# Kernel tuning notes

Measured on AMD Instinct MI355X. Metric: run time of the kernel, lower is better.

Reference implementation:

```python
import jax, jax.numpy as jnp
import numpy as np

NEG_SLOPE = 0.2


def _gat_layer(x, src, dst, W, att_s, att_d, bias):
    # x: [N, F_in]; W: [F_in, H*C]; att_s/att_d: [H, C]; bias: [H*C]
    N = x.shape[0]
    H, C = att_s.shape
    h = (x @ W).reshape(N, H, C)                      # projected features [N,H,C]
    a_src = jnp.einsum('nhc,hc->nh', h, att_s)        # [N,H] per-node src logits
    a_dst = jnp.einsum('nhc,hc->nh', h, att_d)        # [N,H]
    e = a_src[src] + a_dst[dst]                       # [E,H] edge logits
    e = jnp.where(e > 0, e, NEG_SLOPE * e)            # leaky_relu
    # scatter-softmax over incoming edges of each destination node
    m = jax.ops.segment_max(e, dst, num_segments=N)   # [N,H]
    ex = jnp.exp(e - m[dst])                          # [E,H]
    denom = jax.ops.segment_sum(ex, dst, num_segments=N)  # [N,H]
    alpha = ex / denom[dst]                           # [E,H]
    # scatter-add aggregation of weighted source features
    msg = h[src] * alpha[:, :, None]                  # [E,H,C]
    out = jax.ops.segment_sum(msg, dst, num_segments=N)   # [N,H,C]
    return out.reshape(N, H * C) + bias


def _with_self_loops(edge_index, N):
    loop = jnp.arange(N, dtype=edge_index.dtype)
    src = jnp.concatenate([edge_index[0], loop])
    dst = jnp.concatenate([edge_index[1], loop])
    return src, dst


def setup_inputs() -> dict:
    key = jax.random.key(0)
    ks = jax.random.split(key, 10)
    N, E = 50000, 800000
    F_in, C1, H1, F_out = 128, 64, 4, 128
    x = jax.random.normal(ks[0], (N, F_in), dtype=jnp.float32)
    edge_index = jax.random.randint(ks[1], (2, E), 0, N, dtype=jnp.int64)
    s1 = 1.0 / np.sqrt(F_in)
    W1 = jax.random.normal(ks[2], (F_in, H1 * C1), dtype=jnp.float32) * s1
    att_src1 = jax.random.normal(ks[3], (H1, C1), dtype=jnp.float32) * 0.1
    att_dst1 = jax.random.normal(ks[4], (H1, C1), dtype=jnp.float32) * 0.1
    bias1 = jnp.zeros((H1 * C1,), dtype=jnp.float32)
    s2 = 1.0 / np.sqrt(H1 * C1)
    W2 = jax.random.normal(ks[5], (H1 * C1, F_out), dtype=jnp.float32) * s2
    att_src2 = jax.random.normal(ks[6], (1, F_out), dtype=jnp.float32) * 0.1
    att_dst2 = jax.random.normal(ks[7], (1, F_out), dtype=jnp.float32) * 0.1
    bias2 = jnp.zeros((F_out,), dtype=jnp.float32)
    return {"x": x, "edge_index": edge_index,
            "W1": W1, "att_src1": att_src1, "att_dst1": att_dst1, "bias1": bias1,
            "W2": W2, "att_src2": att_src2, "att_dst2": att_dst2, "bias2": bias2}


def reference(x, edge_index, W1, att_src1, att_dst1, bias1,
              W2, att_src2, att_dst2, bias2):
    N = x.shape[0]
    src, dst = _with_self_loops(edge_index, N)
    h1 = _gat_layer(x, src, dst, W1, att_src1, att_dst1, bias1)
    h1 = jax.nn.elu(h1)
    out = _gat_layer(h1, src, dst, W2, att_src2, att_dst2, bias2)
    return out
```

## Files before the change

### kernel.cpp

```cpp
#include <hip/hip_runtime.h>

#define NN 50000
#define NE 800000

constexpr int H1 = 4, F1 = 128, HC1 = 256;
constexpr int HC2 = 128;

typedef unsigned short u16;
typedef unsigned int u32;
typedef __attribute__((ext_vector_type(8))) short bf16x8;
typedef __attribute__((ext_vector_type(4))) float f32x4;

__device__ __forceinline__ float bf2f(u16 h) {
    return __uint_as_float(((u32)h) << 16);
}
__device__ __forceinline__ u16 f2bf(float f) {
    u32 u = __float_as_uint(f);
    u32 r = (u + 0x7fffu + ((u >> 16) & 1u)) >> 16;
    return (u16)r;
}

__device__ __forceinline__ int ld_edge(const int* e32, const long long* e64, int is64, long long idx) {
    return is64 ? (int)e64[idx] : e32[idx];
}

__global__ __launch_bounds__(256) void k_cvt(const float* __restrict__ in, u16* __restrict__ out, int n8) {
    int i = blockIdx.x * 256 + threadIdx.x;
    if (i >= n8) return;
    const float4* p = (const float4*)in + (size_t)i * 2;
    float4 a = p[0], b = p[1];
    ushort4 o0, o1;
    o0.x = f2bf(a.x); o0.y = f2bf(a.y); o0.z = f2bf(a.z); o0.w = f2bf(a.w);
    o1.x = f2bf(b.x); o1.y = f2bf(b.y); o1.z = f2bf(b.z); o1.w = f2bf(b.w);
    ((ushort4*)out)[(size_t)i * 2] = o0;
    ((ushort4*)out)[(size_t)i * 2 + 1] = o1;
}

__global__ void k_zero_detect(int* __restrict__ p, const int* __restrict__ e32, int* __restrict__ flag) {
    int i = blockIdx.x * blockDim.x + threadIdx.x;
    if (i < NN) p[i] = 0;
    if (i == 0) {
        int z = 1;
        for (int t = 0; t < 16; t++)
            if (e32[2 * t + 1] != 0) z = 0;
        *flag = z;
    }
}

__global__ void k_count(const int* __restrict__ e32, const long long* __restrict__ e64,
                        const int* __restrict__ flag, int* __restrict__ deg) {
    int e = blockIdx.x * blockDim.x + threadIdx.x;
    if (e >= NE) return;
    int is64 = *flag;
    int dst = ld_edge(e32, e64, is64, (long long)NE + e);
    atomicAdd(&deg[dst], 1);
}

__global__ __launch_bounds__(256) void k_part(const int* __restrict__ deg, int* __restrict__ bsum) {
    int i = blockIdx.x * 256 + threadIdx.x;
    int v = (i < NN) ? deg[i] : 0;
    #pragma unroll
    for (int off = 1; off < 64; off <<= 1) v += __shfl_xor(v, off);
    __shared__ int ws[4];
    if ((threadIdx.x & 63) == 0) ws[threadIdx.x >> 6] = v;
    __syncthreads();
    if (threadIdx.x == 0) bsum[blockIdx.x] = ws[0] + ws[1] + ws[2] + ws[3];
}

__global__ __launch_bounds__(256) void k_scanb(const int* __restrict__ bsum, int* __restrict__ boff,
                                               int* __restrict__ row_ptr, int NB) {
    const int tid = threadIdx.x;
    const int lane = tid & 63, wv = tid >> 6;
    int v = (tid < NB) ? bsum[tid] : 0;
    int x = v;
    #pragma unroll
    for (int off = 1; off < 64; off <<= 1) {
        int t = __shfl_up(x, off);
        if (lane >= off) x += t;
    }
    __shared__ int wsum[4], woff[4];
    if (lane == 63) wsum[wv] = x;
    __syncthreads();
    if (tid == 0) {
        int run = 0;
        #pragma unroll
        for (int j = 0; j < 4; j++) { woff[j] = run; run += wsum[j]; }
        row_ptr[NN] = run;
    }
    __syncthreads();
    if (tid < NB) boff[tid] = x - v + woff[wv];
}

__global__ __launch_bounds__(256) void k_addb(const int* __restrict__ deg, const int* __restrict__ boff,
                                              int* __restrict__ row_ptr, int* __restrict__ cursor) {
    const int tid = threadIdx.x;
    const int lane = tid & 63, wv = tid >> 6;
    int i = blockIdx.x * 256 + tid;
    int v = (i < NN) ? deg[i] : 0;
    int x = v;
    #pragma unroll
    for (int off = 1; off < 64; off <<= 1) {
        int t = __shfl_up(x, off);
        if (lane >= off) x += t;
    }
    __shared__ int wsum[4], woff[4];
    if (lane == 63) wsum[wv] = x;
    __syncthreads();
    if (tid == 0) {
        int run = 0;
        #pragma unroll
        for (int j = 0; j < 4; j++) { woff[j] = run; run += wsum[j]; }
    }
    __syncthreads();
    int excl = x - v + woff[wv] + boff[blockIdx.x];
    if (i < NN) { row_ptr[i] = excl; cursor[i] = excl; }
}

__global__ void k_fill(const int* __restrict__ e32, const long long* __restrict__ e64,
                       const int* __restrict__ flag, int* __restrict__ cursor, int* __restrict__ col) {
    int e = blockIdx.x * blockDim.x + threadIdx.x;
    if (e >= NE) return;
    int is64 = *flag;
    int src = ld_edge(e32, e64, is64, e);
    int dst = ld_edge(e32, e64, is64, (long long)NE + e);
    int pos = atomicAdd(&cursor[dst], 1);
    col[pos] = src;
}

template <int K, int N>
__global__ __launch_bounds__(256) void k_prepw(const float* __restrict__ W, u16* __restrict__ Wp) {
    constexpr int LGN = (N == 256) ? 8 : 7;
    int o = blockIdx.x * 256 + threadIdx.x;
    if (o >= K * N) return;
    int j = o & 7;
    int lk = (o >> 3) & 3;
    int nn = (o >> 5) & (N - 1);
    int kc = o >> (5 + LGN);
    int k = kc * 32 + lk * 8 + j;
    Wp[o] = f2bf(W[(size_t)k * N + nn]);
}

template <int K, int NOUT, int HEADS, int TPB>
__global__ __launch_bounds__(TPB) void k_gemm_mfma(
    const u16* __restrict__ Ab, const u16* __restrict__ Wp,
    const float* __restrict__ atts, const float* __restrict__ attd,
    u16* __restrict__ Hout, float* __restrict__ as_out, float* __restrict__ ad_out, int M)
{
    constexpr int BM = 64, BK = 32;
    constexpr int NK = K / BK;
    constexpr int C = NOUT / HEADS;
    constexpr int LDA = 40;
    __shared__ __align__(16) u16 As[2][BM * LDA];
    __shared__ float red_s[BM * HEADS];
    __shared__ float red_d[BM * HEADS];

    const int tid = threadIdx.x;
    const int w = tid >> 6;
    const int l = tid & 63;
    const int l15 = l & 15, lk = l >> 4;
    const int row0 = blockIdx.x * BM;
    const int col0 = w * 64;

    for (int i = tid; i < BM * HEADS; i += TPB) { red_s[i] = 0.f; red_d[i] = 0.f; }

    f32x4 acc[4][4];
    #pragma unroll
    for (int rt = 0; rt < 4; rt++)
        #pragma unroll
        for (int nt = 0; nt < 4; nt++)
            acc[rt][nt] = (f32x4){0.f, 0.f, 0.f, 0.f};

    auto stage = [&](int kc, int b) {
        #pragma unroll
        for (int i = tid; i < BM * 4; i += TPB) {
            int r = i >> 2, c = (i & 3) * 8;
            int gr = row0 + r;
            bf16x8 v = {0, 0, 0, 0, 0, 0, 0, 0};
            if (gr < M) v = *(const bf16x8*)(Ab + (size_t)gr * K + kc * BK + c);
            *(bf16x8*)&As[b][r * LDA + c] = v;
        }
    };
    auto loadB = [&](int kc, bf16x8* bf) {
        #pragma unroll
        for (int nt = 0; nt < 4; nt++)
            bf[nt] = *(const bf16x8*)(Wp + (((size_t)kc * NOUT + col0 + nt * 16 + l15) * 4 + lk) * 8);
    };

    bf16x8 bcur[4];
    loadB(0, bcur);
    stage(0, 0);
    for (int kc = 0; kc < NK; ++kc) {
        __syncthreads();
        bf16x8 afr[4];
        #pragma unroll
        for (int rt = 0; rt < 4; rt++)
            afr[rt] = *(const bf16x8*)&As[kc & 1][(rt * 16 + l15) * LDA + lk * 8];
        bf16x8 bnext[4];
        if (kc + 1 < NK) {
            loadB(kc + 1, bnext);
            stage(kc + 1, (kc + 1) & 1);
        }
        #pragma unroll
        for (int rt = 0; rt < 4; rt++)
            #pragma unroll
            for (int nt = 0; nt < 4; nt++)
                acc[rt][nt] = __builtin_amdgcn_mfma_f32_16x16x32_bf16(afr[rt], bcur[nt], acc[rt][nt], 0, 0, 0);
        if (kc + 1 < NK) {
            #pragma unroll
            for (int nt = 0; nt < 4; nt++) bcur[nt] = bnext[nt];
        }
    }

    #pragma unroll
    for (int rt = 0; rt < 4; rt++) {
        #pragma unroll
        for (int t = 0; t < 4; t++) {
            int gr = row0 + rt * 16 + lk * 4 + t;
            if (gr < M) {
                #pragma unroll
                for (int nt = 0; nt < 4; nt++)
                    Hout[(size_t)gr * NOUT + col0 + nt * 16 + l15] = f2bf(acc[rt][nt][t]);
            }
        }
    }

    float avs[4], avd[4];
    #pragma unroll
    for (int nt = 0; nt < 4; nt++) {
        int gc = col0 + nt * 16 + l15;
        avs[nt] = atts[gc];
        avd[nt] = attd[gc];
    }
    const int headw = col0 / C;
    #pragma unroll
    for (int rt = 0; rt < 4; rt++) {
        #pragma unroll
        for (int t = 0; t < 4; t++) {
            float ps = 0.f, pd = 0.f;
            #pragma unroll
            for (int nt = 0; nt < 4; nt++) {
                ps = fmaf(acc[rt][nt][t], avs[nt], ps);
                pd = fmaf(acc[rt][nt][t], avd[nt], pd);
            }
            ps += __shfl_xor(ps, 1); ps += __shfl_xor(ps, 2);
            ps += __shfl_xor(ps, 4); ps += __shfl_xor(ps, 8);
            pd += __shfl_xor(pd, 1); pd += __shfl_xor(pd, 2);
            pd += __shfl_xor(pd, 4); pd += __shfl_xor(pd, 8);
            if (l15 == 0) {
                int row = rt * 16 + lk * 4 + t;
                atomicAdd(&red_s[row * HEADS + headw], ps);
                atomicAdd(&red_d[row * HEADS + headw], pd);
            }
        }
    }
    __syncthreads();
    for (int i = tid; i < BM * HEADS; i += TPB) {
        int gr = row0 + i / HEADS;
        if (gr < M) {
            as_out[(size_t)gr * HEADS + i % HEADS] = red_s[i];
            ad_out[(size_t)gr * HEADS + i % HEADS] = red_d[i];
        }
    }
}

__global__ __launch_bounds__(256) void k_agg1(
    const int* __restrict__ row_ptr, const int* __restrict__ col,
    const u16* __restrict__ Hb, const float* __restrict__ as_, const float* __restrict__ ad_,
    const float* __restrict__ bias, u16* __restrict__ outp)
{
    __shared__ int    s_src[4][64];
    __shared__ float4 s_p[4][64];
    int n = blockIdx.x * 4 + (threadIdx.x >> 6);
    if (n >= NN) return;
    const int lane = threadIdx.x & 63;
    const int wv = threadIdx.x >> 6;
    const int head = lane >> 4;
    float4 ad4 = *(const float4*)(ad_ + (size_t)n * 4);
    int beg = row_ptr[n];
    int cnt = row_ptr[n + 1] - beg + 1;
    float4 sp = make_float4(0.f, 0.f, 0.f, 0.f);
    float ax = 0.f, ay = 0.f, az = 0.f, aw = 0.f;
    for (int c = 0; c < cnt; c += 64) {
        int idx = c + lane;
        int srcl = n;
        float4 p4 = make_float4(0.f, 0.f, 0.f, 0.f);
        if (idx < cnt) {
            srcl = (idx == 0) ? n : col[beg + idx - 1];
            float4 a4 = *(const float4*)(as_ + (size_t)srcl * 4);
            float e;
            e = a4.x + ad4.x; e = e > 0.f ? e : 0.2f * e; p4.x = __expf(e);
            e = a4.y + ad4.y; e = e > 0.f ? e : 0.2f * e; p4.y = __expf(e);
            e = a4.z + ad4.z; e = e > 0.f ? e : 0.2f * e; p4.z = __expf(e);
            e = a4.w + ad4.w; e = e > 0.f ? e : 0.2f * e; p4.w = __expf(e);
        }
        sp.x += p4.x; sp.y += p4.y; sp.z += p4.z; sp.w += p4.w;
        s_src[wv][lane] = srcl;
        s_p[wv][lane] = p4;
        int jmax = min(64, cnt - c);
        #pragma unroll 4
        for (int j = 0; j < jmax; ++j) {
            int srcj = s_src[wv][j];
            float pj = ((const float*)&s_p[wv][j])[head];
            ushort4 hv = *(const ushort4*)(Hb + (size_t)srcj * HC1 + lane * 4);
            ax = fmaf(pj, bf2f(hv.x), ax);
            ay = fmaf(pj, bf2f(hv.y), ay);
            az = fmaf(pj, bf2f(hv.z), az);
            aw = fmaf(pj, bf2f(hv.w), aw);
        }
    }
    #pragma unroll
    for (int off = 1; off < 64; off <<= 1) {
        sp.x += __shfl_xor(sp.x, off);
        sp.y += __shfl_xor(sp.y, off);
        sp.z += __shfl_xor(sp.z, off);
        sp.w += __shfl_xor(sp.w, off);
    }
    float s = head < 2 ? (head == 0 ? sp.x : sp.y) : (head == 2 ? sp.z : sp.w);
    float inv = 1.f / s;
    float4 bv = *(const float4*)(bias + lane * 4);
    float4 o;
    o.x = ax * inv + bv.x;
    o.y = ay * inv + bv.y;
    o.z = az * inv + bv.z;
    o.w = aw * inv + bv.w;
    o.x = o.x > 0.f ? o.x : __expf(o.x) - 1.f;
    o.y = o.y > 0.f ? o.y : __expf(o.y) - 1.f;
    o.z = o.z > 0.f ? o.z : __expf(o.z) - 1.f;
    o.w = o.w > 0.f ? o.w : __expf(o.w) - 1.f;
    ushort4 ob;
    ob.x = f2bf(o.x); ob.y = f2bf(o.y); ob.z = f2bf(o.z); ob.w = f2bf(o.w);
    *(ushort4*)(outp + (size_t)n * HC1 + lane * 4) = ob;
}

__global__ __launch_bounds__(256) void k_agg2(
    const int* __restrict__ row_ptr, const int* __restrict__ col,
    const u16* __restrict__ Hb, const float* __restrict__ as_, const float* __restrict__ ad_,
    const float* __restrict__ bias, float* __restrict__ outp)
{
    __shared__ int   s_src[4][64];
    __shared__ float s_p[4][64];
    int n = blockIdx.x * 4 + (threadIdx.x >> 6);
    if (n >= NN) return;
    const int lane = threadIdx.x & 63;
    const int wv = threadIdx.x >> 6;
    float ad0 = ad_[n];
    int beg = row_ptr[n];
    int cnt = row_ptr[n + 1] - beg + 1;
    float sp = 0.f;
    float ax = 0.f, ay = 0.f;
    for (int c = 0; c < cnt; c += 64) {
        int idx = c + lane;
        int srcl = n;
        float p = 0.f;
        if (idx < cnt) {
            srcl = (idx == 0) ? n : col[beg + idx - 1];
            float e = as_[srcl] + ad0;
            e = e > 0.f ? e : 0.2f * e;
            p = __expf(e);
        }
        sp += p;
        s_src[wv][lane] = srcl;
        s_p[wv][lane] = p;
        int jmax = min(64, cnt - c);
        #pragma unroll 4
        for (int j = 0; j < jmax; ++j) {
            int srcj = s_src[wv][j];
            float pj = s_p[wv][j];
            ushort2 hv = *(const ushort2*)(Hb + (size_t)srcj * HC2 + lane * 2);
            ax = fmaf(pj, bf2f(hv.x), ax);
            ay = fmaf(pj, bf2f(hv.y), ay);
        }
    }
    #pragma unroll
    for (int off = 1; off < 64; off <<= 1) sp += __shfl_xor(sp, off);
    float inv = 1.f / sp;
    float2 bv = *(const float2*)(bias + lane * 2);
    float2 o = make_float2(ax * inv + bv.x, ay * inv + bv.y);
    *(float2*)(outp + (size_t)n * HC2 + lane * 2) = o;
}

extern "C" void kernel_launch(void* const* d_in, const int* in_sizes, int n_in,
                              void* d_out, int out_size, void* d_ws, size_t ws_size,
                              hipStream_t stream) {
    const float* x   = (const float*)d_in[0];
    const int*       e32 = (const int*)d_in[1];
    const long long* e64 = (const long long*)d_in[1];
    const float* W1  = (const float*)d_in[2];
    const float* as1w = (const float*)d_in[3];
    const float* ad1w = (const float*)d_in[4];
    const float* b1  = (const float*)d_in[5];
    const float* W2  = (const float*)d_in[6];
    const float* as2w = (const float*)d_in[7];
    const float* ad2w = (const float*)d_in[8];
    const float* b2  = (const float*)d_in[9];
    float* out = (float*)d_out;

    char* w = (char*)d_ws;
    auto carve = [&](size_t bytes) -> void* {
        void* p = (void*)w;
        w += (bytes + 255) & ~(size_t)255;
        return p;
    };
    int*   flag    = (int*)carve(4);
    int*   row_ptr = (int*)carve((NN + 1) * sizeof(int));
    int*   cursor  = (int*)carve(NN * sizeof(int));
    int*   col     = (int*)carve(NE * sizeof(int));
    int*   bsum    = (int*)carve(256 * sizeof(int));
    int*   boff    = (int*)carve(256 * sizeof(int));
    float* as1     = (float*)carve((size_t)NN * H1 * sizeof(float));
    float* ad1     = (float*)carve((size_t)NN * H1 * sizeof(float));
    float* as2     = (float*)carve((size_t)NN * sizeof(float));
    float* ad2     = (float*)carve((size_t)NN * sizeof(float));
    u16*   xb      = (u16*)carve((size_t)NN * F1 * sizeof(u16));
    u16*   h1b     = (u16*)carve((size_t)NN * HC1 * sizeof(u16));
    u16*   h2in    = (u16*)carve((size_t)NN * HC1 * sizeof(u16));
    u16*   h2b     = (u16*)carve((size_t)NN * HC2 * sizeof(u16));
    u16*   wp1     = (u16*)carve((size_t)F1 * HC1 * sizeof(u16));
    u16*   wp2     = (u16*)carve((size_t)HC1 * HC2 * sizeof(u16));

    const int TPB = 256;
    const int gN  = (NN + TPB - 1) / TPB;
    const int gE  = (NE + TPB - 1) / TPB;
    const int gM  = (NN + 63) / 64;
    const int gAgg = (NN + 3) / 4;

    k_cvt<<<(NN * F1 / 8 + 255) / 256, 256, 0, stream>>>(x, xb, NN * F1 / 8);
    k_prepw<F1, HC1><<<F1 * HC1 / 256, 256, 0, stream>>>(W1, wp1);
    k_prepw<HC1, HC2><<<HC1 * HC2 / 256, 256, 0, stream>>>(W2, wp2);

    k_zero_detect<<<gN, TPB, 0, stream>>>(cursor, e32, flag);
    k_count<<<gE, TPB, 0, stream>>>(e32, e64, flag, cursor);
    k_part<<<gN, TPB, 0, stream>>>(cursor, bsum);
    k_scanb<<<1, 256, 0, stream>>>(bsum, boff, row_ptr, gN);
    k_addb<<<gN, TPB, 0, stream>>>(cursor, boff, row_ptr, cursor);
    k_fill<<<gE, TPB, 0, stream>>>(e32, e64, flag, cursor, col);

    k_gemm_mfma<F1, HC1, H1, 256><<<gM, 256, 0, stream>>>(xb, wp1, as1w, ad1w, h1b, as1, ad1, NN);
    k_agg1<<<gAgg, TPB, 0, stream>>>(row_ptr, col, h1b, as1, ad1, b1, h2in);

    k_gemm_mfma<HC1, HC2, 1, 128><<<gM, 128, 0, stream>>>(h2in, wp2, as2w, ad2w, h2b, as2, ad2, NN);
    k_agg2<<<gAgg, TPB, 0, stream>>>(row_ptr, col, h2b, as2, ad2, b2, out);
}
```

Before: 240.5 us.

## Slice projected features into 32-channel tables and fold self-loops into CSR

The GEMM now writes projected features in a sliced layout of 32-channel tables, each [NN][32]. Aggregation kernels are merged into one template that runs a block per (node group, slice) and processes 8 edges at once per wavefront with sub-lanes, then reduces across sub-groups. Self-loops are now stored directly in the CSR by having the degree start at 1 and writing each node's own id first, which removes the idx==0 branch. This aims to raise gather parallelism and improve cache locality per slice, at the cost of recomputing softmax logits once per slice and adding more blocks plus cross-lane reductions.

```diff
diff --git a/kernel.cpp b/kernel.cpp
--- a/kernel.cpp
+++ b/kernel.cpp
@@ -38,7 +38,7 @@
 
 __global__ void k_zero_detect(int* __restrict__ p, const int* __restrict__ e32, int* __restrict__ flag) {
     int i = blockIdx.x * blockDim.x + threadIdx.x;
-    if (i < NN) p[i] = 0;
+    if (i < NN) p[i] = 1;
     if (i == 0) {
         int z = 1;
         for (int t = 0; t < 16; t++)
@@ -92,7 +92,8 @@
 }
 
 __global__ __launch_bounds__(256) void k_addb(const int* __restrict__ deg, const int* __restrict__ boff,
-                                              int* __restrict__ row_ptr, int* __restrict__ cursor) {
+                                              int* __restrict__ row_ptr, int* __restrict__ cursor,
+                                              int* __restrict__ col) {
     const int tid = threadIdx.x;
     const int lane = tid & 63, wv = tid >> 6;
     int i = blockIdx.x * 256 + tid;
@@ -113,7 +114,11 @@
     }
     __syncthreads();
     int excl = x - v + woff[wv] + boff[blockIdx.x];
-    if (i < NN) { row_ptr[i] = excl; cursor[i] = excl; }
+    if (i < NN) {
+        row_ptr[i] = excl;
+        cursor[i] = excl + 1;
+        col[excl] = i;
+    }
 }
 
 __global__ void k_fill(const int* __restrict__ e32, const long long* __restrict__ e64,
@@ -218,8 +223,10 @@
             int gr = row0 + rt * 16 + lk * 4 + t;
             if (gr < M) {
                 #pragma unroll
-                for (int nt = 0; nt < 4; nt++)
-                    Hout[(size_t)gr * NOUT + col0 + nt * 16 + l15] = f2bf(acc[rt][nt][t]);
+                for (int nt = 0; nt < 4; nt++) {
+                    int c = col0 + nt * 16 + l15;
+                    Hout[((size_t)(c >> 5) * NN + gr) * 32 + (c & 31)] = f2bf(acc[rt][nt][t]);
+                }
             }
         }
     }
@@ -263,120 +270,83 @@
     }
 }
 
-__global__ __launch_bounds__(256) void k_agg1(
-    const int* __restrict__ row_ptr, const int* __restrict__ col,
-    const u16* __restrict__ Hb, const float* __restrict__ as_, const float* __restrict__ ad_,
-    const float* __restrict__ bias, u16* __restrict__ outp)
-{
-    __shared__ int    s_src[4][64];
-    __shared__ float4 s_p[4][64];
-    int n = blockIdx.x * 4 + (threadIdx.x >> 6);
-    if (n >= NN) return;
-    const int lane = threadIdx.x & 63;
-    const int wv = threadIdx.x >> 6;
-    const int head = lane >> 4;
-    float4 ad4 = *(const float4*)(ad_ + (size_t)n * 4);
-    int beg = row_ptr[n];
-    int cnt = row_ptr[n + 1] - beg + 1;
-    float4 sp = make_float4(0.f, 0.f, 0.f, 0.f);
-    float ax = 0.f, ay = 0.f, az = 0.f, aw = 0.f;
-    for (int c = 0; c < cnt; c += 64) {
-        int idx = c + lane;
-        int srcl = n;
-        float4 p4 = make_float4(0.f, 0.f, 0.f, 0.f);
-        if (idx < cnt) {
-            srcl = (idx == 0) ? n : col[beg + idx - 1];
-            float4 a4 = *(const float4*)(as_ + (size_t)srcl * 4);
-            float e;
-            e = a4.x + ad4.x; e = e > 0.f ? e : 0.2f * e; p4.x = __expf(e);
-            e = a4.y + ad4.y; e = e > 0.f ? e : 0.2f * e; p4.y = __expf(e);
-            e = a4.z + ad4.z; e = e > 0.f ? e : 0.2f * e; p4.z = __expf(e);
-            e = a4.w + ad4.w; e = e > 0.f ? e : 0.2f * e; p4.w = __expf(e);
-        }
-        sp.x += p4.x; sp.y += p4.y; sp.z += p4.z; sp.w += p4.w;
-        s_src[wv][lane] = srcl;
-        s_p[wv][lane] = p4;
-        int jmax = min(64, cnt - c);
-        #pragma unroll 4
-        for (int j = 0; j < jmax; ++j) {
-            int srcj = s_src[wv][j];
-            float pj = ((const float*)&s_p[wv][j])[head];
-            ushort4 hv = *(const ushort4*)(Hb + (size_t)srcj * HC1 + lane * 4);
-            ax = fmaf(pj, bf2f(hv.x), ax);
-            ay = fmaf(pj, bf2f(hv.y), ay);
-            az = fmaf(pj, bf2f(hv.z), az);
-            aw = fmaf(pj, bf2f(hv.w), aw);
-        }
-    }
-    #pragma unroll
-    for (int off = 1; off < 64; off <<= 1) {
-        sp.x += __shfl_xor(sp.x, off);
-        sp.y += __shfl_xor(sp.y, off);
-        sp.z += __shfl_xor(sp.z, off);
-        sp.w += __shfl_xor(sp.w, off);
-    }
-    float s = head < 2 ? (head == 0 ? sp.x : sp.y) : (head == 2 ? sp.z : sp.w);
-    float inv = 1.f / s;
-    float4 bv = *(const float4*)(bias + lane * 4);
-    float4 o;
-    o.x = ax * inv + bv.x;
-    o.y = ay * inv + bv.y;
-    o.z = az * inv + bv.z;
-    o.w = aw * inv + bv.w;
-    o.x = o.x > 0.f ? o.x : __expf(o.x) - 1.f;
-    o.y = o.y > 0.f ? o.y : __expf(o.y) - 1.f;
-    o.z = o.z > 0.f ? o.z : __expf(o.z) - 1.f;
-    o.w = o.w > 0.f ? o.w : __expf(o.w) - 1.f;
-    ushort4 ob;
-    ob.x = f2bf(o.x); ob.y = f2bf(o.y); ob.z = f2bf(o.z); ob.w = f2bf(o.w);
-    *(ushort4*)(outp + (size_t)n * HC1 + lane * 4) = ob;
-}
-
-__global__ __launch_bounds__(256) void k_agg2(
-    const int* __restrict__ row_ptr, const int* __restrict__ col,
-    const u16* __restrict__ Hb, const float* __restrict__ as_, const float* __restrict__ ad_,
-    const float* __restrict__ bias, float* __restrict__ outp)
+template <int HCOUT, int NSLICE, int HEADS, int FINAL>
+__global__ __launch_bounds__(256) void k_agg(
+    const int* __restrict__ row_ptr, const int* __restrict__ col, const u16* __restrict__ Hs,
+    const float* __restrict__ as_, const float* __restrict__ ad_,
+    const float* __restrict__ bias, void* __restrict__ outp)
 {
     __shared__ int   s_src[4][64];
     __shared__ float s_p[4][64];
-    int n = blockIdx.x * 4 + (threadIdx.x >> 6);
-    if (n >= NN) return;
-    const int lane = threadIdx.x & 63;
-    const int wv = threadIdx.x >> 6;
-    float ad0 = ad_[n];
+    const int b = blockIdx.x;
+    const int slice = b & (NSLICE - 1);
+    const int nb = b / NSLICE;
+    const int wv = threadIdx.x >> 6, lane = threadIdx.x & 63;
+    const int n = nb * 4 + wv;
+    const int head = (HEADS == 4) ? (slice >> 1) : 0;
+    const int sub = lane >> 3, l8 = lane & 7;
+    const u16* tab = Hs + (size_t)slice * NN * 32;
+
+    float ad0 = ad_[(size_t)n * HEADS + head];
     int beg = row_ptr[n];
-    int cnt = row_ptr[n + 1] - beg + 1;
+    int cnt = row_ptr[n + 1] - beg;
     float sp = 0.f;
-    float ax = 0.f, ay = 0.f;
+    float a0 = 0.f, a1 = 0.f, a2 = 0.f, a3 = 0.f;
     for (int c = 0; c < cnt; c += 64) {
         int idx = c + lane;
-        int srcl = n;
+        int srcl = 0;
         float p = 0.f;
         if (idx < cnt) {
-            srcl = (idx == 0) ? n : col[beg + idx - 1];
-            float e = as_[srcl] + ad0;
+            srcl = __builtin_nontemporal_load(col + beg + idx);
+            float e = as_[(size_t)srcl * HEADS + head] + ad0;
             e = e > 0.f ? e : 0.2f * e;
             p = __expf(e);
         }
         sp += p;
         s_src[wv][lane] = srcl;
         s_p[wv][lane] = p;
-        int jmax = min(64, cnt - c);
-        #pragma unroll 4
-        for (int j = 0; j < jmax; ++j) {
-            int srcj = s_src[wv][j];
-            float pj = s_p[wv][j];
-            ushort2 hv = *(const ushort2*)(Hb + (size_t)srcj * HC2 + lane * 2);
-            ax = fmaf(pj, bf2f(hv.x), ax);
-            ay = fmaf(pj, bf2f(hv.y), ay);
-        }
+        int njit = (min(64, cnt - c) + 7) >> 3;
+        for (int j = 0; j < njit; ++j) {
+            int srcj = s_src[wv][j * 8 + sub];
+            float pj = s_p[wv][j * 8 + sub];
+            ushort4 hv = *(const ushort4*)(tab + (size_t)srcj * 32 + l8 * 4);
+            a0 = fmaf(pj, bf2f(hv.x), a0);
+            a1 = fmaf(pj, bf2f(hv.y), a1);
+            a2 = fmaf(pj, bf2f(hv.z), a2);
+            a3 = fmaf(pj, bf2f(hv.w), a3);
+        }
+    }
+    #pragma unroll
+    for (int off = 8; off <= 32; off <<= 1) {
+        a0 += __shfl_xor(a0, off);
+        a1 += __shfl_xor(a1, off);
+        a2 += __shfl_xor(a2, off);
+        a3 += __shfl_xor(a3, off);
     }
     #pragma unroll
     for (int off = 1; off < 64; off <<= 1) sp += __shfl_xor(sp, off);
-    float inv = 1.f / sp;
-    float2 bv = *(const float2*)(bias + lane * 2);
-    float2 o = make_float2(ax * inv + bv.x, ay * inv + bv.y);
-    *(float2*)(outp + (size_t)n * HC2 + lane * 2) = o;
+
+    if (lane < 8) {
+        float inv = 1.f / sp;
+        int ch = slice * 32 + l8 * 4;
+        float4 bv = *(const float4*)(bias + ch);
+        float4 o;
+        o.x = a0 * inv + bv.x;
+        o.y = a1 * inv + bv.y;
+        o.z = a2 * inv + bv.z;
+        o.w = a3 * inv + bv.w;
+        if (FINAL) {
+            *(float4*)((float*)outp + (size_t)n * HCOUT + ch) = o;
+        } else {
+            o.x = o.x > 0.f ? o.x : __expf(o.x) - 1.f;
+            o.y = o.y > 0.f ? o.y : __expf(o.y) - 1.f;
+            o.z = o.z > 0.f ? o.z : __expf(o.z) - 1.f;
+            o.w = o.w > 0.f ? o.w : __expf(o.w) - 1.f;
+            ushort4 ob;
+            ob.x = f2bf(o.x); ob.y = f2bf(o.y); ob.z = f2bf(o.z); ob.w = f2bf(o.w);
+            *(ushort4*)((u16*)outp + (size_t)n * HCOUT + ch) = ob;
+        }
+    }
 }
 
 extern "C" void kernel_launch(void* const* d_in, const int* in_sizes, int n_in,
@@ -404,7 +374,7 @@
     int*   flag    = (int*)carve(4);
     int*   row_ptr = (int*)carve((NN + 1) * sizeof(int));
     int*   cursor  = (int*)carve(NN * sizeof(int));
-    int*   col     = (int*)carve(NE * sizeof(int));
+    int*   col     = (int*)carve((NE + NN) * sizeof(int));
     int*   bsum    = (int*)carve(256 * sizeof(int));
     int*   boff    = (int*)carve(256 * sizeof(int));
     float* as1     = (float*)carve((size_t)NN * H1 * sizeof(float));
@@ -422,7 +392,6 @@
     const int gN  = (NN + TPB - 1) / TPB;
     const int gE  = (NE + TPB - 1) / TPB;
     const int gM  = (NN + 63) / 64;
-    const int gAgg = (NN + 3) / 4;
 
     k_cvt<<<(NN * F1 / 8 + 255) / 256, 256, 0, stream>>>(x, xb, NN * F1 / 8);
     k_prepw<F1, HC1><<<F1 * HC1 / 256, 256, 0, stream>>>(W1, wp1);
@@ -432,12 +401,12 @@
     k_count<<<gE, TPB, 0, stream>>>(e32, e64, flag, cursor);
     k_part<<<gN, TPB, 0, stream>>>(cursor, bsum);
     k_scanb<<<1, 256, 0, stream>>>(bsum, boff, row_ptr, gN);
-    k_addb<<<gN, TPB, 0, stream>>>(cursor, boff, row_ptr, cursor);
+    k_addb<<<gN, TPB, 0, stream>>>(cursor, boff, row_ptr, cursor, col);
     k_fill<<<gE, TPB, 0, stream>>>(e32, e64, flag, cursor, col);
 
     k_gemm_mfma<F1, HC1, H1, 256><<<gM, 256, 0, stream>>>(xb, wp1, as1w, ad1w, h1b, as1, ad1, NN);
-    k_agg1<<<gAgg, TPB, 0, stream>>>(row_ptr, col, h1b, as1, ad1, b1, h2in);
+    k_agg<HC1, 8, H1, 0><<<(NN / 4) * 8, 256, 0, stream>>>(row_ptr, col, h1b, as1, ad1, b1, h2in);
 
     k_gemm_mfma<HC1, HC2, 1, 128><<<gM, 128, 0, stream>>>(h2in, wp2, as2w, ad2w, h2b, as2, ad2, NN);
-    k_agg2<<<gAgg, TPB, 0, stream>>>(row_ptr, col, h2b, as2, ad2, b2, out);
-}
+    k_agg<HC2, 4, 1, 1><<<(NN / 4) * 4, 256, 0, stream>>>(row_ptr, col, h2b, as2, ad2, b2, out);
+}
```

After: 406.1 us. +68.9%, slower.

## Merge prep kernels, co-schedule CSR fill with GEMM1, widen aggregation gathers

Applied to the files above, without the earlier changes.

Folds the x conversion, both weight repacks and the degree zeroing into one launch, and runs the CSR fill blocks in the same grid as the first GEMM so the two independent stages overlap. The aggregation kernels now have each half-wave process alternate edges with wider per-lane loads (8 bf16 for layer 1, 4 for layer 2), then combine the halves with a cross-half shuffle. This cuts launch count and issued load instructions, at the cost of extra shuffles, idle lanes in the epilogue, and hardcoded block counts that assume NN is divisible by 4.

```diff
diff --git a/kernel.cpp b/kernel.cpp
--- a/kernel.cpp
+++ b/kernel.cpp
@@ -5,6 +5,8 @@
 
 constexpr int H1 = 4, F1 = 128, HC1 = 256;
 constexpr int HC2 = 128;
+constexpr int GM1 = (NN + 63) / 64;
+constexpr int GE  = (NE + 255) / 256;
 
 typedef unsigned short u16;
 typedef unsigned int u32;
@@ -24,26 +26,40 @@
     return is64 ? (int)e64[idx] : e32[idx];
 }
 
-__global__ __launch_bounds__(256) void k_cvt(const float* __restrict__ in, u16* __restrict__ out, int n8) {
-    int i = blockIdx.x * 256 + threadIdx.x;
-    if (i >= n8) return;
-    const float4* p = (const float4*)in + (size_t)i * 2;
-    float4 a = p[0], b = p[1];
-    ushort4 o0, o1;
-    o0.x = f2bf(a.x); o0.y = f2bf(a.y); o0.z = f2bf(a.z); o0.w = f2bf(a.w);
-    o1.x = f2bf(b.x); o1.y = f2bf(b.y); o1.z = f2bf(b.z); o1.w = f2bf(b.w);
-    ((ushort4*)out)[(size_t)i * 2] = o0;
-    ((ushort4*)out)[(size_t)i * 2 + 1] = o1;
-}
-
-__global__ void k_zero_detect(int* __restrict__ p, const int* __restrict__ e32, int* __restrict__ flag) {
-    int i = blockIdx.x * blockDim.x + threadIdx.x;
-    if (i < NN) p[i] = 0;
-    if (i == 0) {
-        int z = 1;
-        for (int t = 0; t < 16; t++)
-            if (e32[2 * t + 1] != 0) z = 0;
-        *flag = z;
+__global__ __launch_bounds__(256) void k_prep(
+    const float* __restrict__ x, const float* __restrict__ W1, const float* __restrict__ W2,
+    u16* __restrict__ xb, u16* __restrict__ wp1, u16* __restrict__ wp2,
+    int* __restrict__ deg, const int* __restrict__ e32, int* __restrict__ flag)
+{
+    const int b = blockIdx.x, tid = threadIdx.x;
+    if (b < 3125) {
+        int i = b * 256 + tid;
+        const float4* p = (const float4*)x + (size_t)i * 2;
+        float4 a = p[0], c = p[1];
+        ushort4 o0, o1;
+        o0.x = f2bf(a.x); o0.y = f2bf(a.y); o0.z = f2bf(a.z); o0.w = f2bf(a.w);
+        o1.x = f2bf(c.x); o1.y = f2bf(c.y); o1.z = f2bf(c.z); o1.w = f2bf(c.w);
+        ((ushort4*)xb)[(size_t)i * 2] = o0;
+        ((ushort4*)xb)[(size_t)i * 2 + 1] = o1;
+    } else if (b < 3253) {
+        int o = (b - 3125) * 256 + tid;
+        int j = o & 7, lk = (o >> 3) & 3, nn = (o >> 5) & 255, kc = o >> 13;
+        int k = kc * 32 + lk * 8 + j;
+        wp1[o] = f2bf(W1[(size_t)k * HC1 + nn]);
+    } else if (b < 3381) {
+        int o = (b - 3253) * 256 + tid;
+        int j = o & 7, lk = (o >> 3) & 3, nn = (o >> 5) & 127, kc = o >> 12;
+        int k = kc * 32 + lk * 8 + j;
+        wp2[o] = f2bf(W2[(size_t)k * HC2 + nn]);
+    } else {
+        int i = (b - 3381) * 256 + tid;
+        if (i < NN) deg[i] = 0;
+        if (b == 3381 && tid == 0) {
+            int z = 1;
+            for (int t = 0; t < 16; t++)
+                if (e32[2 * t + 1] != 0) z = 0;
+            *flag = z;
+        }
     }
 }
 
@@ -116,33 +132,9 @@
     if (i < NN) { row_ptr[i] = excl; cursor[i] = excl; }
 }
 
-__global__ void k_fill(const int* __restrict__ e32, const long long* __restrict__ e64,
-                       const int* __restrict__ flag, int* __restrict__ cursor, int* __restrict__ col) {
-    int e = blockIdx.x * blockDim.x + threadIdx.x;
-    if (e >= NE) return;
-    int is64 = *flag;
-    int src = ld_edge(e32, e64, is64, e);
-    int dst = ld_edge(e32, e64, is64, (long long)NE + e);
-    int pos = atomicAdd(&cursor[dst], 1);
-    col[pos] = src;
-}
-
-template <int K, int N>
-__global__ __launch_bounds__(256) void k_prepw(const float* __restrict__ W, u16* __restrict__ Wp) {
-    constexpr int LGN = (N == 256) ? 8 : 7;
-    int o = blockIdx.x * 256 + threadIdx.x;
-    if (o >= K * N) return;
-    int j = o & 7;
-    int lk = (o >> 3) & 3;
-    int nn = (o >> 5) & (N - 1);
-    int kc = o >> (5 + LGN);
-    int k = kc * 32 + lk * 8 + j;
-    Wp[o] = f2bf(W[(size_t)k * N + nn]);
-}
-
 template <int K, int NOUT, int HEADS, int TPB>
-__global__ __launch_bounds__(TPB) void k_gemm_mfma(
-    const u16* __restrict__ Ab, const u16* __restrict__ Wp,
+__device__ __forceinline__ void gemm_body(
+    int bid, const u16* __restrict__ Ab, const u16* __restrict__ Wp,
     const float* __restrict__ atts, const float* __restrict__ attd,
     u16* __restrict__ Hout, float* __restrict__ as_out, float* __restrict__ ad_out, int M)
 {
@@ -158,7 +150,7 @@
     const int w = tid >> 6;
     const int l = tid & 63;
     const int l15 = l & 15, lk = l >> 4;
-    const int row0 = blockIdx.x * BM;
+    const int row0 = bid * BM;
     const int col0 = w * 64;
 
     for (int i = tid; i < BM * HEADS; i += TPB) { red_s[i] = 0.f; red_d[i] = 0.f; }
@@ -263,6 +255,35 @@
     }
 }
 
+__global__ __launch_bounds__(256) void k_gemm1_fill(
+    const u16* __restrict__ xb, const u16* __restrict__ wp1,
+    const float* __restrict__ as1w, const float* __restrict__ ad1w,
+    u16* __restrict__ h1b, float* __restrict__ as1, float* __restrict__ ad1,
+    const int* __restrict__ e32, const long long* __restrict__ e64,
+    const int* __restrict__ flag, int* __restrict__ cursor, int* __restrict__ col)
+{
+    if (blockIdx.x < GM1) {
+        gemm_body<F1, HC1, H1, 256>(blockIdx.x, xb, wp1, as1w, ad1w, h1b, as1, ad1, NN);
+    } else {
+        int e = (blockIdx.x - GM1) * 256 + threadIdx.x;
+        if (e >= NE) return;
+        int is64 = *flag;
+        int src = ld_edge(e32, e64, is64, e);
+        int dst = ld_edge(e32, e64, is64, (long long)NE + e);
+        int pos = atomicAdd(&cursor[dst], 1);
+        col[pos] = src;
+    }
+}
+
+template <int K, int NOUT, int HEADS, int TPB>
+__global__ __launch_bounds__(TPB) void k_gemm_mfma(
+    const u16* __restrict__ Ab, const u16* __restrict__ Wp,
+    const float* __restrict__ atts, const float* __restrict__ attd,
+    u16* __restrict__ Hout, float* __restrict__ as_out, float* __restrict__ ad_out, int M)
+{
+    gemm_body<K, NOUT, HEADS, TPB>(blockIdx.x, Ab, Wp, atts, attd, Hout, as_out, ad_out, M);
+}
+
 __global__ __launch_bounds__(256) void k_agg1(
     const int* __restrict__ row_ptr, const int* __restrict__ col,
     const u16* __restrict__ Hb, const float* __restrict__ as_, const float* __restrict__ ad_,
@@ -271,43 +292,53 @@
     __shared__ int    s_src[4][64];
     __shared__ float4 s_p[4][64];
     int n = blockIdx.x * 4 + (threadIdx.x >> 6);
-    if (n >= NN) return;
     const int lane = threadIdx.x & 63;
     const int wv = threadIdx.x >> 6;
-    const int head = lane >> 4;
+    const int half = lane >> 5, l32 = lane & 31;
+    const int head8 = l32 >> 3;
     float4 ad4 = *(const float4*)(ad_ + (size_t)n * 4);
     int beg = row_ptr[n];
     int cnt = row_ptr[n + 1] - beg + 1;
     float4 sp = make_float4(0.f, 0.f, 0.f, 0.f);
-    float ax = 0.f, ay = 0.f, az = 0.f, aw = 0.f;
+    float a0 = 0.f, a1 = 0.f, a2 = 0.f, a3 = 0.f;
+    float a4 = 0.f, a5 = 0.f, a6 = 0.f, a7 = 0.f;
     for (int c = 0; c < cnt; c += 64) {
         int idx = c + lane;
         int srcl = n;
         float4 p4 = make_float4(0.f, 0.f, 0.f, 0.f);
         if (idx < cnt) {
             srcl = (idx == 0) ? n : col[beg + idx - 1];
-            float4 a4 = *(const float4*)(as_ + (size_t)srcl * 4);
+            float4 aa = *(const float4*)(as_ + (size_t)srcl * 4);
             float e;
-            e = a4.x + ad4.x; e = e > 0.f ? e : 0.2f * e; p4.x = __expf(e);
-            e = a4.y + ad4.y; e = e > 0.f ? e : 0.2f * e; p4.y = __expf(e);
-            e = a4.z + ad4.z; e = e > 0.f ? e : 0.2f * e; p4.z = __expf(e);
-            e = a4.w + ad4.w; e = e > 0.f ? e : 0.2f * e; p4.w = __expf(e);
+            e = aa.x + ad4.x; e = e > 0.f ? e : 0.2f * e; p4.x = __expf(e);
+            e = aa.y + ad4.y; e = e > 0.f ? e : 0.2f * e; p4.y = __expf(e);
+            e = aa.z + ad4.z; e = e > 0.f ? e : 0.2f * e; p4.z = __expf(e);
+            e = aa.w + ad4.w; e = e > 0.f ? e : 0.2f * e; p4.w = __expf(e);
         }
         sp.x += p4.x; sp.y += p4.y; sp.z += p4.z; sp.w += p4.w;
         s_src[wv][lane] = srcl;
         s_p[wv][lane] = p4;
         int jmax = min(64, cnt - c);
         #pragma unroll 4
-        for (int j = 0; j < jmax; ++j) {
-            int srcj = s_src[wv][j];
-            float pj = ((const float*)&s_p[wv][j])[head];
-            ushort4 hv = *(const ushort4*)(Hb + (size_t)srcj * HC1 + lane * 4);
-            ax = fmaf(pj, bf2f(hv.x), ax);
-            ay = fmaf(pj, bf2f(hv.y), ay);
-            az = fmaf(pj, bf2f(hv.z), az);
-            aw = fmaf(pj, bf2f(hv.w), aw);
-        }
-    }
+        for (int j = 0; j < jmax; j += 2) {
+            int jj = j + half;
+            int srcj = s_src[wv][jj];
+            float pj = ((const float*)&s_p[wv][jj])[head8];
+            bf16x8 hv = *(const bf16x8*)(Hb + (size_t)srcj * HC1 + l32 * 8);
+            a0 = fmaf(pj, bf2f((u16)hv[0]), a0);
+            a1 = fmaf(pj, bf2f((u16)hv[1]), a1);
+            a2 = fmaf(pj, bf2f((u16)hv[2]), a2);
+            a3 = fmaf(pj, bf2f((u16)hv[3]), a3);
+            a4 = fmaf(pj, bf2f((u16)hv[4]), a4);
+            a5 = fmaf(pj, bf2f((u16)hv[5]), a5);
+            a6 = fmaf(pj, bf2f((u16)hv[6]), a6);
+            a7 = fmaf(pj, bf2f((u16)hv[7]), a7);
+        }
+    }
+    a0 += __shfl_xor(a0, 32); a1 += __shfl_xor(a1, 32);
+    a2 += __shfl_xor(a2, 32); a3 += __shfl_xor(a3, 32);
+    a4 += __shfl_xor(a4, 32); a5 += __shfl_xor(a5, 32);
+    a6 += __shfl_xor(a6, 32); a7 += __shfl_xor(a7, 32);
     #pragma unroll
     for (int off = 1; off < 64; off <<= 1) {
         sp.x += __shfl_xor(sp.x, off);
@@ -315,21 +346,31 @@
         sp.z += __shfl_xor(sp.z, off);
         sp.w += __shfl_xor(sp.w, off);
     }
-    float s = head < 2 ? (head == 0 ? sp.x : sp.y) : (head == 2 ? sp.z : sp.w);
-    float inv = 1.f / s;
-    float4 bv = *(const float4*)(bias + lane * 4);
-    float4 o;
-    o.x = ax * inv + bv.x;
-    o.y = ay * inv + bv.y;
-    o.z = az * inv + bv.z;
-    o.w = aw * inv + bv.w;
-    o.x = o.x > 0.f ? o.x : __expf(o.x) - 1.f;
-    o.y = o.y > 0.f ? o.y : __expf(o.y) - 1.f;
-    o.z = o.z > 0.f ? o.z : __expf(o.z) - 1.f;
-    o.w = o.w > 0.f ? o.w : __expf(o.w) - 1.f;
-    ushort4 ob;
-    ob.x = f2bf(o.x); ob.y = f2bf(o.y); ob.z = f2bf(o.z); ob.w = f2bf(o.w);
-    *(ushort4*)(outp + (size_t)n * HC1 + lane * 4) = ob;
+    if (lane < 32) {
+        float s = head8 < 2 ? (head8 == 0 ? sp.x : sp.y) : (head8 == 2 ? sp.z : sp.w);
+        float inv = 1.f / s;
+        int ch0 = l32 * 8;
+        float4 bv0 = *(const float4*)(bias + ch0);
+        float4 bv1 = *(const float4*)(bias + ch0 + 4);
+        float o0 = a0 * inv + bv0.x, o1 = a1 * inv + bv0.y;
+        float o2 = a2 * inv + bv0.z, o3 = a3 * inv + bv0.w;
+        float o4 = a4 * inv + bv1.x, o5 = a5 * inv + bv1.y;
+        float o6 = a6 * inv + bv1.z, o7 = a7 * inv + bv1.w;
+        o0 = o0 > 0.f ? o0 : __expf(o0) - 1.f;
+        o1 = o1 > 0.f ? o1 : __expf(o1) - 1.f;
+        o2 = o2 > 0.f ? o2 : __expf(o2) - 1.f;
+        o3 = o3 > 0.f ? o3 : __expf(o3) - 1.f;
+        o4 = o4 > 0.f ? o4 : __expf(o4) - 1.f;
+        o5 = o5 > 0.f ? o5 : __expf(o5) - 1.f;
+        o6 = o6 > 0.f ? o6 : __expf(o6) - 1.f;
+        o7 = o7 > 0.f ? o7 : __expf(o7) - 1.f;
+        bf16x8 ob;
+        ob[0] = (short)f2bf(o0); ob[1] = (short)f2bf(o1);
+        ob[2] = (short)f2bf(o2); ob[3] = (short)f2bf(o3);
+        ob[4] = (short)f2bf(o4); ob[5] = (short)f2bf(o5);
+        ob[6] = (short)f2bf(o6); ob[7] = (short)f2bf(o7);
+        *(bf16x8*)(outp + (size_t)n * HC1 + ch0) = ob;
+    }
 }
 
 __global__ __launch_bounds__(256) void k_agg2(
@@ -340,14 +381,14 @@
     __shared__ int   s_src[4][64];
     __shared__ float s_p[4][64];
     int n = blockIdx.x * 4 + (threadIdx.x >> 6);
-    if (n >= NN) return;
     const int lane = threadIdx.x & 63;
     const int wv = threadIdx.x >> 6;
+    const int half = lane >> 5, l32 = lane & 31;
     float ad0 = ad_[n];
     int beg = row_ptr[n];
     int cnt = row_ptr[n + 1] - beg + 1;
     float sp = 0.f;
-    float ax = 0.f, ay = 0.f;
+    float a0 = 0.f, a1 = 0.f, a2 = 0.f, a3 = 0.f;
     for (int c = 0; c < cnt; c += 64) {
         int idx = c + lane;
         int srcl = n;
@@ -363,20 +404,32 @@
         s_p[wv][lane] = p;
         int jmax = min(64, cnt - c);
         #pragma unroll 4
-        for (int j = 0; j < jmax; ++j) {
-            int srcj = s_src[wv][j];
-            float pj = s_p[wv][j];
-            ushort2 hv = *(const ushort2*)(Hb + (size_t)srcj * HC2 + lane * 2);
-            ax = fmaf(pj, bf2f(hv.x), ax);
-            ay = fmaf(pj, bf2f(hv.y), ay);
-        }
-    }
+        for (int j = 0; j < jmax; j += 2) {
+            int jj = j + half;
+            int srcj = s_src[wv][jj];
+            float pj = s_p[wv][jj];
+            ushort4 hv = *(const ushort4*)(Hb + (size_t)srcj * HC2 + l32 * 4);
+            a0 = fmaf(pj, bf2f(hv.x), a0);
+            a1 = fmaf(pj, bf2f(hv.y), a1);
+            a2 = fmaf(pj, bf2f(hv.z), a2);
+            a3 = fmaf(pj, bf2f(hv.w), a3);
+        }
+    }
+    a0 += __shfl_xor(a0, 32); a1 += __shfl_xor(a1, 32);
+    a2 += __shfl_xor(a2, 32); a3 += __shfl_xor(a3, 32);
     #pragma unroll
     for (int off = 1; off < 64; off <<= 1) sp += __shfl_xor(sp, off);
-    float inv = 1.f / sp;
-    float2 bv = *(const float2*)(bias + lane * 2);
-    float2 o = make_float2(ax * inv + bv.x, ay * inv + bv.y);
-    *(float2*)(outp + (size_t)n * HC2 + lane * 2) = o;
+    if (lane < 32) {
+        float inv = 1.f / sp;
+        int ch0 = l32 * 4;
+        float4 bv = *(const float4*)(bias + ch0);
+        float4 o;
+        o.x = a0 * inv + bv.x;
+        o.y = a1 * inv + bv.y;
+        o.z = a2 * inv + bv.z;
+        o.w = a3 * inv + bv.w;
+        *(float4*)(outp + (size_t)n * HC2 + ch0) = o;
+    }
 }
 
 extern "C" void kernel_launch(void* const* d_in, const int* in_sizes, int n_in,
@@ -420,24 +473,20 @@
 
     const int TPB = 256;
     const int gN  = (NN + TPB - 1) / TPB;
-    const int gE  = (NE + TPB - 1) / TPB;
-    const int gM  = (NN + 63) / 64;
-    const int gAgg = (NN + 3) / 4;
-
-    k_cvt<<<(NN * F1 / 8 + 255) / 256, 256, 0, stream>>>(x, xb, NN * F1 / 8);
-    k_prepw<F1, HC1><<<F1 * HC1 / 256, 256, 0, stream>>>(W1, wp1);
-    k_prepw<HC1, HC2><<<HC1 * HC2 / 256, 256, 0, stream>>>(W2, wp2);
-
-    k_zero_detect<<<gN, TPB, 0, stream>>>(cursor, e32, flag);
-    k_count<<<gE, TPB, 0, stream>>>(e32, e64, flag, cursor);
+    const int gAgg = NN / 4;
+
+    k_prep<<<3125 + 128 + 128 + 196, 256, 0, stream>>>(x, W1, W2, xb, wp1, wp2, cursor, e32, flag);
+
+    k_count<<<GE, TPB, 0, stream>>>(e32, e64, flag, cursor);
     k_part<<<gN, TPB, 0, stream>>>(cursor, bsum);
     k_scanb<<<1, 256, 0, stream>>>(bsum, boff, row_ptr, gN);
     k_addb<<<gN, TPB, 0, stream>>>(cursor, boff, row_ptr, cursor);
-    k_fill<<<gE, TPB, 0, stream>>>(e32, e64, flag, cursor, col);
-
-    k_gemm_mfma<F1, HC1, H1, 256><<<gM, 256, 0, stream>>>(xb, wp1, as1w, ad1w, h1b, as1, ad1, NN);
+
+    k_gemm1_fill<<<GM1 + GE, 256, 0, stream>>>(xb, wp1, as1w, ad1w, h1b, as1, ad1,
+                                               e32, e64, flag, cursor, col);
+
     k_agg1<<<gAgg, TPB, 0, stream>>>(row_ptr, col, h1b, as1, ad1, b1, h2in);
 
-    k_gemm_mfma<HC1, HC2, 1, 128><<<gM, 128, 0, stream>>>(h2in, wp2, as2w, ad2w, h2b, as2, ad2, NN);
+    k_gemm_mfma<HC1, HC2, 1, 128><<<GM1, 128, 0, stream>>>(h2in, wp2, as2w, ad2w, h2b, as2, ad2, NN);
     k_agg2<<<gAgg, TPB, 0, stream>>>(row_ptr, col, h2b, as2, ad2, b2, out);
 }
```

New measurement: 238.6 us. About the same (-0.8%).
